# Performance work log

Measured on AMD Instinct MI355X. Metric: run time of the kernel, lower is better.

The kernel has to match this reference:

```python
import jax, jax.numpy as jnp
import numpy as np

N_NODES = 20000
IN_FEAT = 128
CONV_OUT = 32
N_EDGES = 640000
FC1_OUT = 128


def setup_inputs() -> dict:
    key = jax.random.key(0)
    ks = jax.random.split(key, 8)
    x = jax.random.normal(ks[0], (N_NODES, IN_FEAT), dtype=jnp.float32)
    edge_index = jax.random.randint(ks[1], (2, N_EDGES), 0, N_NODES, dtype=jnp.int64)
    # GCNConv params (PyG: lin weight [in, out] applied as x @ W, plus bias)
    w_conv = jax.random.normal(ks[2], (IN_FEAT, CONV_OUT), dtype=jnp.float32) * (1.0 / np.sqrt(IN_FEAT))
    b_conv = jnp.zeros((CONV_OUT,), dtype=jnp.float32)
    # fc1: Linear(32*N -> 128), torch stores weight as [out, in]
    w_fc1 = jax.random.normal(ks[3], (FC1_OUT, CONV_OUT * N_NODES), dtype=jnp.float32) * (1.0 / np.sqrt(CONV_OUT * N_NODES))
    b_fc1 = jnp.zeros((FC1_OUT,), dtype=jnp.float32)
    # fc2: Linear(128 -> N)
    w_fc2 = jax.random.normal(ks[4], (N_NODES, FC1_OUT), dtype=jnp.float32) * (1.0 / np.sqrt(FC1_OUT))
    b_fc2 = jnp.zeros((N_NODES,), dtype=jnp.float32)
    return {"x": x, "edge_index": edge_index, "w_conv": w_conv, "b_conv": b_conv,
            "w_fc1": w_fc1, "b_fc1": b_fc1, "w_fc2": w_fc2, "b_fc2": b_fc2}


def gcn_conv(x, edge_index, w, b):
    # PyG GCNConv default: add self-loops, symmetric normalization D^-1/2 (A+I) D^-1/2
    n = x.shape[0]
    loop = jnp.arange(n, dtype=edge_index.dtype)
    src = jnp.concatenate([edge_index[0], loop])  # [E+N]
    dst = jnp.concatenate([edge_index[1], loop])
    deg = jax.ops.segment_sum(jnp.ones_like(dst, dtype=x.dtype), dst, num_segments=n)
    dinv = jnp.where(deg > 0, jax.lax.rsqrt(deg), 0.0)
    norm = dinv[src] * dinv[dst]  # [E+N]
    h = x @ w  # [N, out] — transform before propagate
    msg = h[src] * norm[:, None]  # gather
    agg = jax.ops.segment_sum(msg, dst, num_segments=n)  # scatter-add
    return agg + b


def reference(x, edge_index, w_conv, b_conv, w_fc1, b_fc1, w_fc2, b_fc2):
    h1 = jax.nn.relu(gcn_conv(x, edge_index, w_conv, b_conv))  # [N, 32]; dropout inactive (eval)
    flat = h1.reshape(-1, CONV_OUT * N_NODES)  # [1, 32*N]
    h3 = jax.nn.relu(flat @ w_fc1.T + b_fc1)   # [1, 128]
    out = jax.nn.relu(h3 @ w_fc2.T + b_fc2)    # [1, N] q-values
    return out
```

## Files before the change

kernel.cpp:

```cpp
#include <hip/hip_runtime.h>

#define N_NODES 20000
#define IN_FEAT 128
#define CONV_OUT 32
#define N_EDGES 640000
#define FC1_OUT 128


#define ZERO_WORDS 40128

__global__ __launch_bounds__(256) void k_zero(float4* __restrict__ p) {
    int i = blockIdx.x * 256 + threadIdx.x;
    if (i < ZERO_WORDS / 4) p[i] = make_float4(0.f, 0.f, 0.f, 0.f);
}

__global__ __launch_bounds__(256) void k_degi(const int* __restrict__ ei, int* __restrict__ cnt) {
    int e = blockIdx.x * 256 + threadIdx.x;
    if (e < N_EDGES) {
        int s = ei[e];
        int d = ei[N_EDGES + e];
        if ((unsigned)s < N_NODES && (unsigned)d < N_NODES) atomicAdd(&cnt[d], 1);
    }
}

#define SCAN_CHUNK 20
__global__ __launch_bounds__(1024) void k_scan(int* __restrict__ cnt ,
                                               int* __restrict__ cursor,
                                               float* __restrict__ dinv) {
    __shared__ int ps[1024];
    int t = threadIdx.x;
    int base = t * SCAN_CHUNK;
    int local[SCAN_CHUNK];
    int sum = 0;
    #pragma unroll
    for (int i = 0; i < SCAN_CHUNK; ++i) {
        int n = base + i;
        int v = (n < N_NODES) ? cnt[n] : 0;
        local[i] = v;
        sum += v;
    }
    ps[t] = sum;
    __syncthreads();
    #pragma unroll
    for (int off = 1; off < 1024; off <<= 1) {
        int v = (t >= off) ? ps[t - off] : 0;
        __syncthreads();
        ps[t] += v;
        __syncthreads();
    }
    int run = (t == 0) ? 0 : ps[t - 1];
    #pragma unroll
    for (int i = 0; i < SCAN_CHUNK; ++i) {
        int n = base + i;
        if (n < N_NODES) {
            cnt[n] = run;
            cursor[n] = run;
            dinv[n] = rsqrtf((float)local[i] + 1.0f);
            run += local[i];
        }
    }
}

__global__ __launch_bounds__(256) void k_gemm1(const float* __restrict__ x,
                                               const float* __restrict__ w,
                                               const float* __restrict__ dinv,
                                               float* __restrict__ h) {
    __shared__ float xs[64][132];
    __shared__ float ws[128][32];
    int tid = threadIdx.x;
    int n0 = blockIdx.x * 64;

    const float4* w4 = (const float4*)w;
    float4* ws4 = (float4*)ws;
    #pragma unroll
    for (int i = 0; i < 4; ++i) ws4[i * 256 + tid] = w4[i * 256 + tid];

    const float4* x4 = (const float4*)x;
    #pragma unroll
    for (int i = 0; i < 8; ++i) {
        int idx = i * 256 + tid;
        int nl  = idx >> 5;
        int k4  = idx & 31;
        int n   = n0 + nl;
        float4 v = make_float4(0.f, 0.f, 0.f, 0.f);
        if (n < N_NODES) v = x4[(size_t)n * 32 + k4];
        *(float4*)&xs[nl][k4 * 4] = v;
    }
    __syncthreads();

    int c4  = tid & 7;
    int nl0 = tid >> 3;
    const float4* wsrow = (const float4*)ws;
    #pragma unroll
    for (int p = 0; p < 2; ++p) {
        int nl = nl0 + p * 32;
        float4 acc = make_float4(0.f, 0.f, 0.f, 0.f);
        #pragma unroll 8
        for (int k = 0; k < 128; k += 4) {
            float4 xv  = *(const float4*)&xs[nl][k];
            float4 wv0 = wsrow[(k + 0) * 8 + c4];
            float4 wv1 = wsrow[(k + 1) * 8 + c4];
            float4 wv2 = wsrow[(k + 2) * 8 + c4];
            float4 wv3 = wsrow[(k + 3) * 8 + c4];
            acc.x += xv.x * wv0.x + xv.y * wv1.x + xv.z * wv2.x + xv.w * wv3.x;
            acc.y += xv.x * wv0.y + xv.y * wv1.y + xv.z * wv2.y + xv.w * wv3.y;
            acc.z += xv.x * wv0.z + xv.y * wv1.z + xv.z * wv2.z + xv.w * wv3.z;
            acc.w += xv.x * wv0.w + xv.y * wv1.w + xv.z * wv2.w + xv.w * wv3.w;
        }
        int n = n0 + nl;
        if (n < N_NODES) {
            float dv = dinv[n];
            acc.x *= dv; acc.y *= dv; acc.z *= dv; acc.w *= dv;
            *(float4*)&h[(size_t)n * 32 + c4 * 4] = acc;
        }
    }
}

__global__ __launch_bounds__(256) void k_fill(const int* __restrict__ ei,
                                              int* __restrict__ cursor,
                                              int* __restrict__ csr) {
    int e = blockIdx.x * 256 + threadIdx.x;
    if (e < N_EDGES) {
        int s = ei[e];
        int d = ei[N_EDGES + e];
        if ((unsigned)s < N_NODES && (unsigned)d < N_NODES) {
            int pos = atomicAdd(&cursor[d], 1);
            csr[pos] = s;
        }
    }
}

__global__ __launch_bounds__(256) void k_gather(const int* __restrict__ startv,
                                                const int* __restrict__ endv,
                                                const int* __restrict__ csr,
                                                const float* __restrict__ h,
                                                const float* __restrict__ dinv,
                                                const float* __restrict__ bc,
                                                float* __restrict__ flat) {
    int tid  = threadIdx.x;
    int lane = tid & 63;
    int n    = blockIdx.x * 4 + (tid >> 6);
    if (n >= N_NODES) return;
    int es = lane >> 3;
    int f4 = lane & 7;
    const float4* h4 = (const float4*)h;
    float4 acc = make_float4(0.f, 0.f, 0.f, 0.f);
    int p0 = startv[n], p1 = endv[n];
    #pragma unroll 2
    for (int p = p0 + es; p < p1; p += 8) {
        int s = csr[p];
        float4 v = h4[(size_t)s * 8 + f4];
        acc.x += v.x; acc.y += v.y; acc.z += v.z; acc.w += v.w;
    }
    #pragma unroll
    for (int m = 8; m < 64; m <<= 1) {
        acc.x += __shfl_xor(acc.x, m);
        acc.y += __shfl_xor(acc.y, m);
        acc.z += __shfl_xor(acc.z, m);
        acc.w += __shfl_xor(acc.w, m);
    }
    if (lane < 8) {
        float4 self = h4[(size_t)n * 8 + f4];
        float dv = dinv[n];
        float4 b = ((const float4*)bc)[f4];
        float4 r;
        r.x = fmaxf((acc.x + self.x) * dv + b.x, 0.f);
        r.y = fmaxf((acc.y + self.y) * dv + b.y, 0.f);
        r.z = fmaxf((acc.z + self.z) * dv + b.z, 0.f);
        r.w = fmaxf((acc.w + self.w) * dv + b.w, 0.f);
        ((float4*)flat)[(size_t)n * 8 + f4] = r;
    }
}

__global__ __launch_bounds__(256) void k_fc1(const float* __restrict__ flat,
                                             const float* __restrict__ w,
                                             float* __restrict__ h3pre) {
    int bid = blockIdx.x;
    int j  = bid & 127;
    int ch = bid >> 7;
    const float4* w4 = (const float4*)(w + (size_t)j * (CONV_OUT * N_NODES));
    const float4* f4 = (const float4*)flat;
    int base = ch * 6400;
    float acc = 0.f;
    #pragma unroll 5
    for (int it = 0; it < 25; ++it) {
        int k = base + it * 256 + threadIdx.x;
        float4 wv = w4[k];
        float4 fv = f4[k];
        acc += wv.x * fv.x + wv.y * fv.y + wv.z * fv.z + wv.w * fv.w;
    }
    #pragma unroll
    for (int o = 32; o > 0; o >>= 1) acc += __shfl_down(acc, o);
    __shared__ float red[4];
    if ((threadIdx.x & 63) == 0) red[threadIdx.x >> 6] = acc;
    __syncthreads();
    if (threadIdx.x == 0) atomicAdd(&h3pre[j], red[0] + red[1] + red[2] + red[3]);
}

__global__ __launch_bounds__(256) void k_fc2(const float* __restrict__ h3pre,
                                             const float* __restrict__ b1,
                                             const float* __restrict__ w2,
                                             const float* __restrict__ b2,
                                             float* __restrict__ out) {
    __shared__ float4 h3s[32];
    int tid = threadIdx.x;
    if (tid < 32) {
        float4 v;
        v.x = fmaxf(h3pre[tid * 4 + 0] + b1[tid * 4 + 0], 0.f);
        v.y = fmaxf(h3pre[tid * 4 + 1] + b1[tid * 4 + 1], 0.f);
        v.z = fmaxf(h3pre[tid * 4 + 2] + b1[tid * 4 + 2], 0.f);
        v.w = fmaxf(h3pre[tid * 4 + 3] + b1[tid * 4 + 3], 0.f);
        h3s[tid] = v;
    }
    __syncthreads();
    int i = blockIdx.x * 256 + tid;
    if (i < N_NODES) {
        const float4* wr = (const float4*)(w2 + (size_t)i * FC1_OUT);
        float acc = b2[i];
        #pragma unroll
        for (int j = 0; j < 32; ++j) {
            float4 wv = wr[j];
            float4 hv = h3s[j];
            acc += wv.x * hv.x + wv.y * hv.y + wv.z * hv.z + wv.w * hv.w;
        }
        out[i] = fmaxf(acc, 0.f);
    }
}

extern "C" void kernel_launch(void* const* d_in, const int* in_sizes, int n_in,
                              void* d_out, int out_size, void* d_ws, size_t ws_size,
                              hipStream_t stream) {
    const float* x      = (const float*)d_in[0];
    const int*   ei     = (const int*)d_in[1];
    const float* w_conv = (const float*)d_in[2];
    const float* b_conv = (const float*)d_in[3];
    const float* w_fc1  = (const float*)d_in[4];
    const float* b_fc1  = (const float*)d_in[5];
    const float* w_fc2  = (const float*)d_in[6];
    const float* b_fc2  = (const float*)d_in[7];
    float* ws = (float*)d_ws;
    int*   startv = (int*)ws;
    int*   cursor = (int*)(ws + 20000);
    float* h3pre  = ws + 40000;
    float* dinv   = ws + 40128;
    int*   csr    = (int*)(ws + 60128);
    float* h      = ws + 700128;
    float* flat   = ws + 1340128;
    float* out    = (float*)d_out;

    k_zero<<<(ZERO_WORDS / 4 + 255) / 256, 256, 0, stream>>>((float4*)d_ws);
    k_degi<<<(N_EDGES + 255) / 256, 256, 0, stream>>>(ei, startv);
    k_scan<<<1, 1024, 0, stream>>>(startv, cursor, dinv);
    k_gemm1<<<(N_NODES + 63) / 64, 256, 0, stream>>>(x, w_conv, dinv, h);
    k_fill<<<(N_EDGES + 255) / 256, 256, 0, stream>>>(ei, cursor, csr);
    k_gather<<<(N_NODES + 3) / 4, 256, 0, stream>>>(startv, cursor, csr, h, dinv, b_conv, flat);
    k_fc1<<<128 * 25, 256, 0, stream>>>(flat, w_fc1, h3pre);
    k_fc2<<<(N_NODES + 255) / 256, 256, 0, stream>>>(h3pre, b_fc1, w_fc2, b_fc2, out);
}
```

Measured before the change: 203.3 us.

## Record per-edge slot during degree count to remove atomics from CSR fill

The degree-counting kernel now stores the return value of its atomicAdd as a per-edge slot index. The fill kernel then writes each edge to startv[d]+r[e] with no second atomic pass and no cursor array. The scan stages counts through shared memory with vectorized loads and stores, and writes an end sentinel so the gather kernel reads start[n+1] instead of a separate end array. This costs an extra 640K-int array of writes and reads, and drops the bounds checks on edge indices.

```diff
diff --git a/kernel.cpp b/kernel.cpp
--- a/kernel.cpp
+++ b/kernel.cpp
@@ -7,42 +7,47 @@
 #define FC1_OUT 128
 
 
-#define ZERO_WORDS 40128
+#define ZERO_WORDS 20128
 
 __global__ __launch_bounds__(256) void k_zero(float4* __restrict__ p) {
     int i = blockIdx.x * 256 + threadIdx.x;
     if (i < ZERO_WORDS / 4) p[i] = make_float4(0.f, 0.f, 0.f, 0.f);
 }
 
-__global__ __launch_bounds__(256) void k_degi(const int* __restrict__ ei, int* __restrict__ cnt) {
+__global__ __launch_bounds__(256) void k_degslot(const int* __restrict__ ei,
+                                                 int* __restrict__ cnt,
+                                                 int* __restrict__ r) {
     int e = blockIdx.x * 256 + threadIdx.x;
     if (e < N_EDGES) {
-        int s = ei[e];
         int d = ei[N_EDGES + e];
-        if ((unsigned)s < N_NODES && (unsigned)d < N_NODES) atomicAdd(&cnt[d], 1);
-    }
-}
-
+        r[e] = atomicAdd(&cnt[d], 1);
+    }
+}
+
+#define SCAN_T 1024
 #define SCAN_CHUNK 20
-__global__ __launch_bounds__(1024) void k_scan(int* __restrict__ cnt ,
-                                               int* __restrict__ cursor,
+__global__ __launch_bounds__(1024) void k_scan(const int* __restrict__ cnt,
+                                               int* __restrict__ startv,
                                                float* __restrict__ dinv) {
-    __shared__ int ps[1024];
+    __shared__ int ld[SCAN_T * SCAN_CHUNK];
+    __shared__ int ps[SCAN_T];
     int t = threadIdx.x;
+    const int4* c4 = (const int4*)cnt;
+    int4* l4 = (int4*)ld;
+    #pragma unroll
+    for (int i = 0; i < 5; ++i) {
+        int idx = i * SCAN_T + t;
+        l4[idx] = (idx < N_NODES / 4) ? c4[idx] : make_int4(0, 0, 0, 0);
+    }
+    __syncthreads();
+    int local[SCAN_CHUNK];
     int base = t * SCAN_CHUNK;
-    int local[SCAN_CHUNK];
     int sum = 0;
     #pragma unroll
-    for (int i = 0; i < SCAN_CHUNK; ++i) {
-        int n = base + i;
-        int v = (n < N_NODES) ? cnt[n] : 0;
-        local[i] = v;
-        sum += v;
-    }
+    for (int i = 0; i < SCAN_CHUNK; ++i) { local[i] = ld[base + i]; sum += local[i]; }
     ps[t] = sum;
     __syncthreads();
-    #pragma unroll
-    for (int off = 1; off < 1024; off <<= 1) {
+    for (int off = 1; off < SCAN_T; off <<= 1) {
         int v = (t >= off) ? ps[t - off] : 0;
         __syncthreads();
         ps[t] += v;
@@ -52,13 +57,18 @@
     #pragma unroll
     for (int i = 0; i < SCAN_CHUNK; ++i) {
         int n = base + i;
-        if (n < N_NODES) {
-            cnt[n] = run;
-            cursor[n] = run;
-            dinv[n] = rsqrtf((float)local[i] + 1.0f);
-            run += local[i];
-        }
-    }
+        ld[n] = run;
+        if (n < N_NODES) dinv[n] = rsqrtf((float)local[i] + 1.0f);
+        run += local[i];
+    }
+    __syncthreads();
+    int4* s4 = (int4*)startv;
+    #pragma unroll
+    for (int i = 0; i < 5; ++i) {
+        int idx = i * SCAN_T + t;
+        if (idx < N_NODES / 4) s4[idx] = l4[idx];
+    }
+    if (t == 0) startv[N_NODES] = N_EDGES;
 }
 
 __global__ __launch_bounds__(256) void k_gemm1(const float* __restrict__ x,
@@ -117,21 +127,18 @@
 }
 
 __global__ __launch_bounds__(256) void k_fill(const int* __restrict__ ei,
-                                              int* __restrict__ cursor,
+                                              const int* __restrict__ startv,
+                                              const int* __restrict__ r,
                                               int* __restrict__ csr) {
     int e = blockIdx.x * 256 + threadIdx.x;
     if (e < N_EDGES) {
         int s = ei[e];
         int d = ei[N_EDGES + e];
-        if ((unsigned)s < N_NODES && (unsigned)d < N_NODES) {
-            int pos = atomicAdd(&cursor[d], 1);
-            csr[pos] = s;
-        }
+        csr[startv[d] + r[e]] = s;
     }
 }
 
 __global__ __launch_bounds__(256) void k_gather(const int* __restrict__ startv,
-                                                const int* __restrict__ endv,
                                                 const int* __restrict__ csr,
                                                 const float* __restrict__ h,
                                                 const float* __restrict__ dinv,
@@ -145,7 +152,7 @@
     int f4 = lane & 7;
     const float4* h4 = (const float4*)h;
     float4 acc = make_float4(0.f, 0.f, 0.f, 0.f);
-    int p0 = startv[n], p1 = endv[n];
+    int p0 = startv[n], p1 = startv[n + 1];
     #pragma unroll 2
     for (int p = p0 + es; p < p1; p += 8) {
         int s = csr[p];
@@ -163,12 +170,12 @@
         float4 self = h4[(size_t)n * 8 + f4];
         float dv = dinv[n];
         float4 b = ((const float4*)bc)[f4];
-        float4 r;
-        r.x = fmaxf((acc.x + self.x) * dv + b.x, 0.f);
-        r.y = fmaxf((acc.y + self.y) * dv + b.y, 0.f);
-        r.z = fmaxf((acc.z + self.z) * dv + b.z, 0.f);
-        r.w = fmaxf((acc.w + self.w) * dv + b.w, 0.f);
-        ((float4*)flat)[(size_t)n * 8 + f4] = r;
+        float4 r_;
+        r_.x = fmaxf((acc.x + self.x) * dv + b.x, 0.f);
+        r_.y = fmaxf((acc.y + self.y) * dv + b.y, 0.f);
+        r_.z = fmaxf((acc.z + self.z) * dv + b.z, 0.f);
+        r_.w = fmaxf((acc.w + self.w) * dv + b.w, 0.f);
+        ((float4*)flat)[(size_t)n * 8 + f4] = r_;
     }
 }
 
@@ -239,21 +246,22 @@
     const float* w_fc2  = (const float*)d_in[6];
     const float* b_fc2  = (const float*)d_in[7];
     float* ws = (float*)d_ws;
-    int*   startv = (int*)ws;
-    int*   cursor = (int*)(ws + 20000);
-    float* h3pre  = ws + 40000;
-    float* dinv   = ws + 40128;
-    int*   csr    = (int*)(ws + 60128);
-    float* h      = ws + 700128;
-    float* flat   = ws + 1340128;
+    int*   cnt    = (int*)ws;
+    float* h3pre  = ws + 20000;
+    int*   startv = (int*)(ws + 20128);
+    float* dinv   = ws + 40132;
+    int*   r      = (int*)(ws + 60132);
+    int*   csr    = (int*)(ws + 700132);
+    float* h      = ws + 1340132;
+    float* flat   = ws + 1980132;
     float* out    = (float*)d_out;
 
     k_zero<<<(ZERO_WORDS / 4 + 255) / 256, 256, 0, stream>>>((float4*)d_ws);
-    k_degi<<<(N_EDGES + 255) / 256, 256, 0, stream>>>(ei, startv);
-    k_scan<<<1, 1024, 0, stream>>>(startv, cursor, dinv);
+    k_degslot<<<(N_EDGES + 255) / 256, 256, 0, stream>>>(ei, cnt, r);
+    k_scan<<<1, SCAN_T, 0, stream>>>(cnt, startv, dinv);
     k_gemm1<<<(N_NODES + 63) / 64, 256, 0, stream>>>(x, w_conv, dinv, h);
-    k_fill<<<(N_EDGES + 255) / 256, 256, 0, stream>>>(ei, cursor, csr);
-    k_gather<<<(N_NODES + 3) / 4, 256, 0, stream>>>(startv, cursor, csr, h, dinv, b_conv, flat);
+    k_fill<<<(N_EDGES + 255) / 256, 256, 0, stream>>>(ei, startv, r, csr);
+    k_gather<<<(N_NODES + 3) / 4, 256, 0, stream>>>(startv, csr, h, dinv, b_conv, flat);
     k_fc1<<<128 * 25, 256, 0, stream>>>(flat, w_fc1, h3pre);
     k_fc2<<<(N_NODES + 255) / 256, 256, 0, stream>>>(h3pre, b_fc1, w_fc2, b_fc2, out);
 }
```

Result: faster. 164.9 us (-18.9%).
